# Performance work log

Hardware: AMD Instinct MI355X
Metric: run time of the kernel (lower is better)

The kernel has to match this reference:

```python
import jax, jax.numpy as jnp
import numpy as np
import math

NUM_CLUSTERS = 3


def _maxpool_last(x, k=9, pad=4):
    # torch MaxPool with default stride=kernel_size; pad positions are -inf
    nd = x.ndim
    return jax.lax.reduce_window(
        x, -jnp.inf, jax.lax.max,
        (1,) * (nd - 1) + (k,),
        (1,) * (nd - 1) + (k,),
        [(0, 0)] * (nd - 1) + [(pad, pad)],
    )


def setup_inputs() -> dict:
    key = jax.random.key(0)
    ks = jax.random.split(key, 8)
    b, h, l, dk = 36, 8, 1152, 72
    dm = h * dk  # 576 == d_model
    c = NUM_CLUSTERS
    f = lambda k_, sh: jax.random.normal(k_, sh, jnp.float32)
    return {
        "Q": f(ks[0], (b, h, l, dk)),
        "K": f(ks[1], (b, h, l, dk)),
        "V": f(ks[2], (b, h, l, dk)),
        "Wp": f(ks[3], (dm, c)) * 0.05, "bp": jnp.zeros((c,), jnp.float32),
        "Wck": f(ks[4], (c, c)) * 0.5, "bck": jnp.zeros((c,), jnp.float32),
        "Wcq": f(ks[5], (c, c)) * 0.5, "bcq": jnp.zeros((c,), jnp.float32),
        "Wb": f(ks[6], (c, dm)) * 0.05, "bb": jnp.zeros((dm,), jnp.float32),
    }


def reference(Q, K, V, Wp, bp, Wck, bck, Wcq, bcq, Wb, bb):
    b, h, l, dk = Q.shape
    dm = h * dk
    c = NUM_CLUSTERS
    b2 = b // 2

    # MaxPool1d(kernel=9, stride=9, pad=4) applied to raw reshape (b, dk*h, l)
    Kp = _maxpool_last(K.reshape(b, dm, l)).reshape(b, h, -1, dk)
    Vp = _maxpool_last(V.reshape(b, dm, l)).reshape(b, h, -1, dk)
    l_k = Kp.shape[2]

    # pad batch dim with zeros, then unfold dim0 with window b/2, step 1
    K_padded = jnp.concatenate(
        [jnp.zeros((b2, h, l_k, dk), Q.dtype), Kp[1:]], axis=0)  # (b2+b-1, h, l_k, dk)
    idx = jnp.arange(b)[:, None] + jnp.arange(b2)[None, :]  # (b, b2)
    # torch unfold puts window dim last: (b, h, l_k, dk, b2)
    K_unf = jnp.transpose(K_padded[idx], (0, 2, 3, 4, 1)).reshape(b, l_k, b2, dm)

    cluster_k_p = jax.nn.relu(K_unf @ Wp + bp)          # (b, l_k, b2, c)
    cluster_k = jax.nn.softmax(cluster_k_p @ Wck + bck, axis=-1)
    cluster_q = jax.nn.softmax(cluster_k_p @ Wcq + bcq, axis=-1)

    mu = jnp.mean(cluster_q, axis=-1)                    # (b, l_k, b2)
    sigma = jax.nn.softplus(jnp.std(cluster_q, axis=-1, ddof=1))  # torch std unbiased
    xk = jnp.mean(cluster_k, axis=-1)
    log_prob = (-0.5 * jnp.square((xk - mu) / sigma)
                - jnp.log(sigma) - 0.5 * math.log(2.0 * math.pi))
    # CrossEntropyLoss(mu, mu): soft targets over class dim 1 (l_k), mean over rest
    ce = jnp.mean(-jnp.sum(mu * jax.nn.log_softmax(mu, axis=1), axis=1))
    loss = -jnp.mean(log_prob) + ce

    scores = jnp.einsum('blpc,bluc->blpu', cluster_q, cluster_k) / c  # (b,l_k,b2,b2)
    mask = jnp.triu(jnp.ones((b2, b2), bool), k=1)
    scores = jnp.where(mask, jnp.float32(-1e9), scores)
    attn = jax.nn.softmax(scores, axis=-1)
    cluster_q2 = jnp.einsum('blpu,bluc->blpc', attn, cluster_q)       # (b,l_k,b2,c)

    cluster_center = jax.nn.relu(cluster_q2 @ Wb + bb)                # (b,l_k,b2,dm)
    # MaxPool2d(kernel=(1,9), stride=(1,9), pad=(0,4)) over last dim
    cluster_center = _maxpool_last(cluster_center)                    # (b,l_k,b2,ceil(dm/9))
    cluster_center = cluster_center.reshape(b, h, -1, l_k, dk)        # raw reshape

    scores_center = jnp.einsum('bhqd,bhckd->bhqk', Q, cluster_center)  # (b,h,l,l_k)
    attn2 = jax.nn.softmax(scores_center, axis=-1)
    context = jnp.einsum('bhqk,bhkd->bhqd', attn2, Vp)
    return context, loss
```

## Files before the change

### kernel.cpp

```cpp
#include <hip/hip_runtime.h>
#include <math.h>

#define BATCH 36
#define H 8
#define L 1152
#define DK 72
#define DM 576
#define LK 128
#define B2 18
#define NC 3

#define POOL_PER_B (DM*LK)
#define POOL_TOTAL (BATCH*POOL_PER_B)
#define CLUS_TOTAL (BATCH*LK*B2)
#define CTX_ELEMS (BATCH*H*L*DK)
#define NBH (BATCH*H)
#define CFRAG_T (NBH*8*3*64)
#define VFRAG_T (NBH*5*4*64)

typedef __attribute__((ext_vector_type(8))) short short8;
typedef __attribute__((ext_vector_type(4))) float f32x4;

__device__ __forceinline__ unsigned short bf16_rne(float x) {
  unsigned u = __float_as_uint(x);
  unsigned r = u + 0x7FFFu + ((u >> 16) & 1u);
  return (unsigned short)(r >> 16);
}
__device__ __forceinline__ unsigned pack2(float a, float b) {
  return (unsigned)bf16_rne(a) | ((unsigned)bf16_rne(b) << 16);
}
__device__ __forceinline__ float max9(float x0, float x1, float x2, float x3,
                                      float x4, float x5, float x6, float x7,
                                      float x8) {
  float m0 = fmaxf(fmaxf(x0, x1), x2);
  float m1 = fmaxf(fmaxf(x3, x4), x5);
  float m2 = fmaxf(fmaxf(x6, x7), x8);
  return fmaxf(fmaxf(m0, m1), m2);
}

__global__ __launch_bounds__(256, 8) void pool_kernel(
    const float* __restrict__ Kin, const float* __restrict__ Vin,
    float* __restrict__ pK, uint2* __restrict__ Vfrag2) {
  int t = blockIdx.x * 256 + threadIdx.x;
  const int perT = (BATCH * DM) * 32;
  bool isK = t < perT;
  const float* src;
  if (isK) {
    src = Kin;
  } else {
    src = Vin; t -= perT;
  }
  int row = t >> 5, g = t & 31;
  const float* p = src + (size_t)row * L + g * 36;

  float4 a[9];
#pragma unroll
  for (int k = 0; k < 8; ++k) a[k + 1] = *(const float4*)(p + k * 4);
  a[0] = (g > 0) ? *(const float4*)(p - 4)
                 : make_float4(-INFINITY, -INFINITY, -INFINITY, -INFINITY);
  __builtin_amdgcn_sched_barrier(0);

  float w0 = max9(a[0].x, a[0].y, a[0].z, a[0].w,
                  a[1].x, a[1].y, a[1].z, a[1].w, a[2].x);
  float w1 = max9(a[2].y, a[2].z, a[2].w,
                  a[3].x, a[3].y, a[3].z, a[3].w, a[4].x, a[4].y);
  float w2 = max9(a[4].z, a[4].w,
                  a[5].x, a[5].y, a[5].z, a[5].w, a[6].x, a[6].y, a[6].z);
  float w3 = max9(a[6].w,
                  a[7].x, a[7].y, a[7].z, a[7].w,
                  a[8].x, a[8].y, a[8].z, a[8].w);

  if (isK) {
    *(float4*)(pK + (size_t)row * LK + g * 4) = make_float4(w0, w1, w2, w3);
  } else {
    int bb = row / DM, m = row % DM;
    int hh = m / DK, d = m % DK;
    int bh = bb * 8 + hh;
    int nt = d >> 4, dl = d & 15;
    int ks = g >> 3, sub = (g & 7) >> 1, half = g & 1;
    int lane = (sub << 4) | dl;
    size_t u4 = (((size_t)bh * 5 + nt) * 4 + ks) * 64 + lane;
    Vfrag2[u4 * 2 + half] = make_uint2(pack2(w0, w1), pack2(w2, w3));
  }
}

__global__ __launch_bounds__(256) void cluster_kernel(
    const float* __restrict__ pK,
    const float* __restrict__ Wp,  const float* __restrict__ bp,
    const float* __restrict__ Wck, const float* __restrict__ bck,
    const float* __restrict__ Wcq, const float* __restrict__ bcq,
    float* __restrict__ cq_out, float* __restrict__ ck_out,
    float* __restrict__ loss_acc) {
  int bb = blockIdx.x / 9;
  int s  = blockIdx.x % 9;
  int tid = threadIdx.x;

  __shared__ float sK[256 * 33];
  __shared__ float sWp[1728];
  __shared__ float red[256];

  for (int i = tid; i < 1728; i += 256) sWp[i] = Wp[i];

  float a0 = 0.f, a1 = 0.f, a2 = 0.f;
  int umin = (bb >= 18) ? 0 : (18 - bb);

  for (int u = umin; u < 18; ++u) {
    int b2 = bb + u - 17;
    __syncthreads();
    const float4* src = (const float4*)(pK + (size_t)b2 * POOL_PER_B + s * 8192);
#pragma unroll
    for (int k = 0; k < 8; ++k) {
      int i = tid + k * 256;
      float4 v = src[i];
      int base = i * 4;
      float* dst = &sK[(base >> 5) * 33 + (base & 31)];
      dst[0] = v.x; dst[1] = v.y; dst[2] = v.z; dst[3] = v.w;
    }
    __syncthreads();
    const float* wrow = &sWp[u * 3];
    const float* krow = &sK[tid * 33];
#pragma unroll
    for (int g = 0; g < 32; ++g) {
      float v = krow[g];
      a0 = fmaf(v, wrow[g * 54 + 0], a0);
      a1 = fmaf(v, wrow[g * 54 + 1], a1);
      a2 = fmaf(v, wrow[g * 54 + 2], a2);
    }
  }

  float p0 = fmaxf(a0 + bp[0], 0.f);
  float p1 = fmaxf(a1 + bp[1], 0.f);
  float p2 = fmaxf(a2 + bp[2], 0.f);

  float k0 = p0 * Wck[0] + p1 * Wck[3] + p2 * Wck[6] + bck[0];
  float k1 = p0 * Wck[1] + p1 * Wck[4] + p2 * Wck[7] + bck[1];
  float k2 = p0 * Wck[2] + p1 * Wck[5] + p2 * Wck[8] + bck[2];
  float mk = fmaxf(k0, fmaxf(k1, k2));
  float e0 = __expf(k0 - mk), e1 = __expf(k1 - mk), e2 = __expf(k2 - mk);
  float inv = 1.f / (e0 + e1 + e2);
  float ck0 = e0 * inv, ck1 = e1 * inv, ck2 = e2 * inv;

  float q0 = p0 * Wcq[0] + p1 * Wcq[3] + p2 * Wcq[6] + bcq[0];
  float q1 = p0 * Wcq[1] + p1 * Wcq[4] + p2 * Wcq[7] + bcq[1];
  float q2 = p0 * Wcq[2] + p1 * Wcq[5] + p2 * Wcq[8] + bcq[2];
  float mq = fmaxf(q0, fmaxf(q1, q2));
  float f0 = __expf(q0 - mq), f1 = __expf(q1 - mq), f2 = __expf(q2 - mq);
  float invq = 1.f / (f0 + f1 + f2);
  float cq0 = f0 * invq, cq1 = f1 * invq, cq2 = f2 * invq;

  size_t t = (size_t)bb * 2304 + s * 256 + tid;
  ck_out[t * 3 + 0] = ck0;
  ck_out[t * 3 + 1] = ck1;
  ck_out[t * 3 + 2] = ck2;
  cq_out[t * 3 + 0] = cq0;
  cq_out[t * 3 + 1] = cq1;
  cq_out[t * 3 + 2] = cq2;

  float mean = (cq0 + cq1 + cq2) * (1.f / 3.f);
  float d0 = cq0 - mean, d1 = cq1 - mean, d2 = cq2 - mean;
  float var = (d0 * d0 + d1 * d1 + d2 * d2) * 0.5f;
  float sd  = sqrtf(var);
  float sig = log1pf(__expf(sd));
  float ls  = logf(sig);

  __syncthreads();
  red[tid] = ls;
  __syncthreads();
  for (int r = 128; r > 0; r >>= 1) {
    if (tid < r) red[tid] += red[tid + r];
    __syncthreads();
  }
  if (tid == 0) atomicAdd(loss_acc, red[0]);
}

__global__ __launch_bounds__(256) void center2_kernel(
    const float* __restrict__ cq, const float* __restrict__ ck,
    const float* __restrict__ Wb, const float* __restrict__ bbias,
    uint4* __restrict__ Cfrag) {
  int bid = blockIdx.x;
  int mt = bid & 7, hh = (bid >> 3) & 7, bb = bid >> 6;
  int L0 = hh * 16 + mt;
  int tid = threadIdx.x;

  __shared__ float sWb[1728];
  __shared__ float sbb[576];
  __shared__ float scq[2][54], sck[2][54], sq2[2][54];
  __shared__ float pooled[2][1152];

  for (int i = tid; i < 1728; i += 256) sWb[i] = Wb[i];
  for (int i = tid; i < 576; i += 256) sbb[i] = bbias[i];
  if (tid < 108) {
    int h2 = tid / 54, r = tid % 54;
    int Lx = L0 + h2 * 8;
    const float* cqb = cq + ((size_t)bb * 2304 + Lx * 18) * 3;
    const float* ckb = ck + ((size_t)bb * 2304 + Lx * 18) * 3;
    scq[h2][r] = cqb[r];
    sck[h2][r] = ckb[r];
  }
  __syncthreads();

  {
    int h2 = tid >> 6;
    int p  = tid & 63;
    if (h2 < 2 && p < B2) {
      float s[B2];
      float g0 = scq[h2][p * 3 + 0], g1 = scq[h2][p * 3 + 1], g2 = scq[h2][p * 3 + 2];
      float mx = -INFINITY;
#pragma unroll
      for (int u = 0; u < B2; ++u) {
        float sv = (g0 * sck[h2][u * 3] + g1 * sck[h2][u * 3 + 1] +
                    g2 * sck[h2][u * 3 + 2]) * (1.f / 3.f);
        if (u > p) sv = -1e9f;
        s[u] = sv;
        mx = fmaxf(mx, sv);
      }
      float sum = 0.f;
#pragma unroll
      for (int u = 0; u < B2; ++u) { s[u] = __expf(s[u] - mx); sum += s[u]; }
      float inv = 1.f / sum;
      float o0 = 0.f, o1 = 0.f, o2 = 0.f;
#pragma unroll
      for (int u = 0; u < B2; ++u) {
        float a = s[u] * inv;
        o0 = fmaf(a, scq[h2][u * 3 + 0], o0);
        o1 = fmaf(a, scq[h2][u * 3 + 1], o1);
        o2 = fmaf(a, scq[h2][u * 3 + 2], o2);
      }
      sq2[h2][p * 3 + 0] = o0; sq2[h2][p * 3 + 1] = o1; sq2[h2][p * 3 + 2] = o2;
    }
  }
  __syncthreads();

  for (int i = tid; i < 2 * 1152; i += 256) {
    int h2 = i / 1152, r = i % 1152;
    int p = r >> 6, w = r & 63;
    float g0 = sq2[h2][p * 3 + 0], g1 = sq2[h2][p * 3 + 1], g2 = sq2[h2][p * 3 + 2];
    int t0 = w * 9 - 4;
    int lo = t0 < 0 ? 0 : t0;
    int hi = t0 + 8; if (hi > 575) hi = 575;
    float mxv = -INFINITY;
    for (int tt = lo; tt <= hi; ++tt) {
      float cv = g0 * sWb[tt] + g1 * sWb[576 + tt] + g2 * sWb[1152 + tt] + sbb[tt];
      cv = fmaxf(cv, 0.f);
      mxv = fmaxf(mxv, cv);
    }
    pooled[h2][r] = mxv;
  }
  __syncthreads();

  if (tid < 192) {
    int ks = tid >> 6, lane = tid & 63;
    int kk = lane & 15;
    int d0 = ks * 32 + ((lane >> 4) << 3);
    unsigned short hi8[8];
#pragma unroll
    for (int j = 0; j < 8; ++j) {
      int d = d0 + j;
      float v = 0.f;
      if (d < 72) {
        int idx = kk * 72 + d;
        v = pooled[0][idx] + pooled[1][idx];
      }
      hi8[j] = bf16_rne(v);
    }
    uint4 h4;
    h4.x = hi8[0] | (hi8[1] << 16); h4.y = hi8[2] | (hi8[3] << 16);
    h4.z = hi8[4] | (hi8[5] << 16); h4.w = hi8[6] | (hi8[7] << 16);
    int bh = bb * 8 + hh;
    Cfrag[(((size_t)bh * 8 + mt) * 3 + ks) * 64 + lane] = h4;
  }
}

__global__ __launch_bounds__(256) void attn2_kernel(
    const float* __restrict__ Q, const uint4* __restrict__ Cfrag,
    const uint4* __restrict__ Vfrag, float* __restrict__ out,
    const float* __restrict__ loss_acc, float* __restrict__ out_loss) {
  __shared__ __align__(16) uint4 sFrag[2816];

  if (blockIdx.x == 0 && threadIdx.x == 0)
    *out_loss = loss_acc[0] * (1.f / 82944.f) + 207.93889646f;

  int bh = blockIdx.x / 9, qt = blockIdx.x % 9;
  int tid = threadIdx.x;
  int wid = tid >> 6, lane = tid & 63;
  int lq = lane & 15, lg = lane >> 4;
  int qbase = qt * 128 + wid * 32;

  const uint4* gC = Cfrag + (size_t)bh * 1536;
  const uint4* gV = Vfrag + (size_t)bh * 1280;
#pragma unroll
  for (int k = 0; k < 6; ++k) sFrag[tid + k * 256] = gC[tid + k * 256];
#pragma unroll
  for (int k = 0; k < 5; ++k) sFrag[1536 + tid + k * 256] = gV[tid + k * 256];
  __syncthreads();

  f32x4 sacc[2][8];
#pragma unroll
  for (int s = 0; s < 2; ++s)
#pragma unroll
    for (int mt = 0; mt < 8; ++mt) sacc[s][mt] = (f32x4){0.f, 0.f, 0.f, 0.f};

#pragma unroll
  for (int ks = 0; ks < 3; ++ks) {
    short8 qh[2];
#pragma unroll
    for (int s = 0; s < 2; ++s) {
      int q = qbase + s * 16 + lq;
      const float* qrow = Q + ((size_t)bh * L + q) * DK;
      int d0 = ks * 32 + lg * 8;
      float x[8];
      if (ks < 2) {
        float4 a = *(const float4*)(qrow + d0);
        float4 b = *(const float4*)(qrow + d0 + 4);
        x[0] = a.x; x[1] = a.y; x[2] = a.z; x[3] = a.w;
        x[4] = b.x; x[5] = b.y; x[6] = b.z; x[7] = b.w;
      } else {
        if (lg == 0) {
          float4 a = *(const float4*)(qrow + 64);
          float4 b = *(const float4*)(qrow + 68);
          x[0] = a.x; x[1] = a.y; x[2] = a.z; x[3] = a.w;
          x[4] = b.x; x[5] = b.y; x[6] = b.z; x[7] = b.w;
        } else {
#pragma unroll
          for (int j = 0; j < 8; ++j) x[j] = 0.f;
        }
      }
#pragma unroll
      for (int j = 0; j < 8; ++j) qh[s][j] = (short)bf16_rne(x[j]);
    }
#pragma unroll
    for (int mt = 0; mt < 8; ++mt) {
      short8 chi = *(const short8*)&sFrag[(mt * 3 + ks) * 64 + lane];
#pragma unroll
      for (int s = 0; s < 2; ++s)
        sacc[s][mt] = __builtin_amdgcn_mfma_f32_16x16x32_bf16(chi, qh[s], sacc[s][mt], 0, 0, 0);
    }
  }

  unsigned pw[2][8][2];
#pragma unroll
  for (int s = 0; s < 2; ++s) {
    float mx = -INFINITY;
#pragma unroll
    for (int mt = 0; mt < 8; ++mt)
#pragma unroll
      for (int r = 0; r < 4; ++r) mx = fmaxf(mx, sacc[s][mt][r]);
    mx = fmaxf(mx, __shfl_xor(mx, 16));
    mx = fmaxf(mx, __shfl_xor(mx, 32));
    float sum = 0.f;
#pragma unroll
    for (int mt = 0; mt < 8; ++mt)
#pragma unroll
      for (int r = 0; r < 4; ++r) {
        float p = __expf(sacc[s][mt][r] - mx);
        sacc[s][mt][r] = p;
        sum += p;
      }
    sum += __shfl_xor(sum, 16);
    sum += __shfl_xor(sum, 32);
    float inv = 1.f / sum;
#pragma unroll
    for (int mt = 0; mt < 8; ++mt) {
      pw[s][mt][0] = pack2(sacc[s][mt][0] * inv, sacc[s][mt][1] * inv);
      pw[s][mt][1] = pack2(sacc[s][mt][2] * inv, sacc[s][mt][3] * inv);
    }
  }

  f32x4 oacc[2][5];
#pragma unroll
  for (int s = 0; s < 2; ++s)
#pragma unroll
    for (int nt = 0; nt < 5; ++nt) oacc[s][nt] = (f32x4){0.f, 0.f, 0.f, 0.f};

  int baseA = lq + 32 * (lg & 1);
  int baseB = baseA + 16;
  bool hiGrp = (lg & 2) != 0;

#pragma unroll
  for (int ks = 0; ks < 4; ++ks) {
    short8 pa[2];
#pragma unroll
    for (int s = 0; s < 2; ++s) {
      unsigned a0 = pw[s][2 * ks][0],     a1 = pw[s][2 * ks][1];
      unsigned b0 = pw[s][2 * ks + 1][0], b1 = pw[s][2 * ks + 1][1];
      unsigned r00 = __shfl(a0, baseA, 64), r10 = __shfl(b0, baseA, 64);
      unsigned r01 = __shfl(a1, baseA, 64), r11 = __shfl(b1, baseA, 64);
      unsigned r02 = __shfl(a0, baseB, 64), r12 = __shfl(b0, baseB, 64);
      unsigned r03 = __shfl(a1, baseB, 64), r13 = __shfl(b1, baseB, 64);
      uint4 u;
      u.x = hiGrp ? r10 : r00;
      u.y = hiGrp ? r11 : r01;
      u.z = hiGrp ? r12 : r02;
      u.w = hiGrp ? r13 : r03;
      pa[s] = *(short8*)&u;
    }
#pragma unroll
    for (int nt = 0; nt < 5; ++nt) {
      short8 vhi = *(const short8*)&sFrag[1536 + (nt * 4 + ks) * 64 + lane];
#pragma unroll
      for (int s = 0; s < 2; ++s)
        oacc[s][nt] = __builtin_amdgcn_mfma_f32_16x16x32_bf16(pa[s], vhi, oacc[s][nt], 0, 0, 0);
    }
  }

#pragma unroll
  for (int s = 0; s < 2; ++s) {
#pragma unroll
    for (int nt = 0; nt < 5; ++nt) {
      int d = nt * 16 + lq;
      if (d < 72) {
        float* orow = out + ((size_t)bh * L + qbase + s * 16 + lg * 4) * DK + d;
#pragma unroll
        for (int r = 0; r < 4; ++r) orow[(size_t)r * DK] = oacc[s][nt][r];
      }
    }
  }
}

extern "C" void kernel_launch(void* const* d_in, const int* in_sizes, int n_in,
                              void* d_out, int out_size, void* d_ws, size_t ws_size,
                              hipStream_t stream) {
  const float* Q    = (const float*)d_in[0];
  const float* Kin  = (const float*)d_in[1];
  const float* Vin  = (const float*)d_in[2];
  const float* Wp   = (const float*)d_in[3];
  const float* bp   = (const float*)d_in[4];
  const float* Wck  = (const float*)d_in[5];
  const float* bck  = (const float*)d_in[6];
  const float* Wcq  = (const float*)d_in[7];
  const float* bcq  = (const float*)d_in[8];
  const float* Wb   = (const float*)d_in[9];
  const float* bbv  = (const float*)d_in[10];
  float* out = (float*)d_out;

  float* ws = (float*)d_ws;
  float* pK       = ws;
  float* cq       = pK + POOL_TOTAL;
  float* ck       = cq + (size_t)CLUS_TOTAL * 3;
  uint4* Cfrag    = (uint4*)(ck + (size_t)CLUS_TOTAL * 3);
  uint4* Vfrag    = Cfrag + (size_t)CFRAG_T;
  float* loss_acc = (float*)(Vfrag + (size_t)VFRAG_T);

  hipMemsetAsync(loss_acc, 0, sizeof(float), stream);
  hipMemsetAsync(Vfrag, 0, (size_t)VFRAG_T * sizeof(uint4), stream);

  pool_kernel<<<2 * (BATCH * DM) * 32 / 256, 256, 0, stream>>>(
      Kin, Vin, pK, (uint2*)Vfrag);
  cluster_kernel<<<BATCH * 9, 256, 0, stream>>>(
      pK, Wp, bp, Wck, bck, Wcq, bcq, cq, ck, loss_acc);
  center2_kernel<<<BATCH * 64, 256, 0, stream>>>(cq, ck, Wb, bbv, Cfrag);
  attn2_kernel<<<NBH * 9, 256, 0, stream>>>(
      Q, Cfrag, Vfrag, out, loss_acc, out + CTX_ELEMS);
}
```

Measured before the change: 180.4 us.

## Split K/V pooling and overlap V pooling with cluster kernel

The combined K/V max-pool kernel is split. K pooling runs alone first, and V pooling is folded into the cluster kernel as extra trailing blocks. The V pooling blocks, which are bandwidth-bound, can then run alongside the latency-bound cluster blocks and fill idle CUs. The cost is a larger launch for the cluster kernel with mixed block types, whose shared-memory use may limit how many V-pool blocks fit on a CU at once.

```diff
diff --git a/kernel.cpp b/kernel.cpp
--- a/kernel.cpp
+++ b/kernel.cpp
@@ -17,6 +17,8 @@
 #define NBH (BATCH*H)
 #define CFRAG_T (NBH*8*3*64)
 #define VFRAG_T (NBH*5*4*64)
+#define GROUPS_PER_T ((BATCH*DM)*32)
+#define POOL_BLOCKS (GROUPS_PER_T/256)
 
 typedef __attribute__((ext_vector_type(8))) short short8;
 typedef __attribute__((ext_vector_type(4))) float f32x4;
@@ -38,41 +40,52 @@
   return fmaxf(fmaxf(m0, m1), m2);
 }
 
-__global__ __launch_bounds__(256, 8) void pool_kernel(
-    const float* __restrict__ Kin, const float* __restrict__ Vin,
-    float* __restrict__ pK, uint2* __restrict__ Vfrag2) {
-  int t = blockIdx.x * 256 + threadIdx.x;
-  const int perT = (BATCH * DM) * 32;
-  bool isK = t < perT;
-  const float* src;
-  if (isK) {
-    src = Kin;
-  } else {
-    src = Vin; t -= perT;
-  }
-  int row = t >> 5, g = t & 31;
+__device__ __forceinline__ void pool_group(const float* __restrict__ src,
+                                           int row, int g,
+                                           float& w0, float& w1,
+                                           float& w2, float& w3) {
   const float* p = src + (size_t)row * L + g * 36;
-
   float4 a[9];
 #pragma unroll
   for (int k = 0; k < 8; ++k) a[k + 1] = *(const float4*)(p + k * 4);
   a[0] = (g > 0) ? *(const float4*)(p - 4)
                  : make_float4(-INFINITY, -INFINITY, -INFINITY, -INFINITY);
   __builtin_amdgcn_sched_barrier(0);
-
-  float w0 = max9(a[0].x, a[0].y, a[0].z, a[0].w,
-                  a[1].x, a[1].y, a[1].z, a[1].w, a[2].x);
-  float w1 = max9(a[2].y, a[2].z, a[2].w,
-                  a[3].x, a[3].y, a[3].z, a[3].w, a[4].x, a[4].y);
-  float w2 = max9(a[4].z, a[4].w,
-                  a[5].x, a[5].y, a[5].z, a[5].w, a[6].x, a[6].y, a[6].z);
-  float w3 = max9(a[6].w,
-                  a[7].x, a[7].y, a[7].z, a[7].w,
-                  a[8].x, a[8].y, a[8].z, a[8].w);
-
-  if (isK) {
-    *(float4*)(pK + (size_t)row * LK + g * 4) = make_float4(w0, w1, w2, w3);
-  } else {
+  w0 = max9(a[0].x, a[0].y, a[0].z, a[0].w,
+            a[1].x, a[1].y, a[1].z, a[1].w, a[2].x);
+  w1 = max9(a[2].y, a[2].z, a[2].w,
+            a[3].x, a[3].y, a[3].z, a[3].w, a[4].x, a[4].y);
+  w2 = max9(a[4].z, a[4].w,
+            a[5].x, a[5].y, a[5].z, a[5].w, a[6].x, a[6].y, a[6].z);
+  w3 = max9(a[6].w,
+            a[7].x, a[7].y, a[7].z, a[7].w,
+            a[8].x, a[8].y, a[8].z, a[8].w);
+}
+
+__global__ __launch_bounds__(256, 8) void poolk_kernel(
+    const float* __restrict__ Kin, float* __restrict__ pK) {
+  int t = blockIdx.x * 256 + threadIdx.x;
+  int row = t >> 5, g = t & 31;
+  float w0, w1, w2, w3;
+  pool_group(Kin, row, g, w0, w1, w2, w3);
+  *(float4*)(pK + (size_t)row * LK + g * 4) = make_float4(w0, w1, w2, w3);
+}
+
+__global__ __launch_bounds__(256) void cluster_poolv_kernel(
+    const float* __restrict__ pK, const float* __restrict__ Vin,
+    uint2* __restrict__ Vfrag2,
+    const float* __restrict__ Wp,  const float* __restrict__ bp,
+    const float* __restrict__ Wck, const float* __restrict__ bck,
+    const float* __restrict__ Wcq, const float* __restrict__ bcq,
+    float* __restrict__ cq_out, float* __restrict__ ck_out,
+    float* __restrict__ loss_acc) {
+  int tid = threadIdx.x;
+
+  if (blockIdx.x >= BATCH * 9) {
+    int t = (blockIdx.x - BATCH * 9) * 256 + tid;
+    int row = t >> 5, g = t & 31;
+    float w0, w1, w2, w3;
+    pool_group(Vin, row, g, w0, w1, w2, w3);
     int bb = row / DM, m = row % DM;
     int hh = m / DK, d = m % DK;
     int bh = bb * 8 + hh;
@@ -81,19 +94,11 @@
     int lane = (sub << 4) | dl;
     size_t u4 = (((size_t)bh * 5 + nt) * 4 + ks) * 64 + lane;
     Vfrag2[u4 * 2 + half] = make_uint2(pack2(w0, w1), pack2(w2, w3));
-  }
-}
-
-__global__ __launch_bounds__(256) void cluster_kernel(
-    const float* __restrict__ pK,
-    const float* __restrict__ Wp,  const float* __restrict__ bp,
-    const float* __restrict__ Wck, const float* __restrict__ bck,
-    const float* __restrict__ Wcq, const float* __restrict__ bcq,
-    float* __restrict__ cq_out, float* __restrict__ ck_out,
-    float* __restrict__ loss_acc) {
+    return;
+  }
+
   int bb = blockIdx.x / 9;
   int s  = blockIdx.x % 9;
-  int tid = threadIdx.x;
 
   __shared__ float sK[256 * 33];
   __shared__ float sWp[1728];
@@ -444,10 +449,9 @@
   hipMemsetAsync(loss_acc, 0, sizeof(float), stream);
   hipMemsetAsync(Vfrag, 0, (size_t)VFRAG_T * sizeof(uint4), stream);
 
-  pool_kernel<<<2 * (BATCH * DM) * 32 / 256, 256, 0, stream>>>(
-      Kin, Vin, pK, (uint2*)Vfrag);
-  cluster_kernel<<<BATCH * 9, 256, 0, stream>>>(
-      pK, Wp, bp, Wck, bck, Wcq, bcq, cq, ck, loss_acc);
+  poolk_kernel<<<POOL_BLOCKS, 256, 0, stream>>>(Kin, pK);
+  cluster_poolv_kernel<<<BATCH * 9 + POOL_BLOCKS, 256, 0, stream>>>(
+      pK, Vin, (uint2*)Vfrag, Wp, bp, Wck, bck, Wcq, bcq, cq, ck, loss_acc);
   center2_kernel<<<BATCH * 64, 256, 0, stream>>>(cq, ck, Wb, bbv, Cfrag);
   attn2_kernel<<<NBH * 9, 256, 0, stream>>>(
       Q, Cfrag, Vfrag, out, loss_acc, out + CTX_ELEMS);
```

Result: faster. 171.2 us (-5.1%).
